# Optimization experiments

Hardware: AMD Instinct MI355X
Metric: run time of the kernel (lower is better)

The kernel has to match this reference:

```python
import jax, jax.numpy as jnp
import numpy as np

L, D, H, DR, KF = 2, 256, 8, 64, 4   # n_layer, d_model, n_head, d_rpe, k_feedforward
B, S, T = 2, 256, 256
LN_EPS = 1e-5


def _ln(x, g, b):
    m = jnp.mean(x, -1, keepdims=True)
    v = jnp.mean((x - m) ** 2, -1, keepdims=True)
    return (x - m) * jax.lax.rsqrt(v + LN_EPS) * g + b


def _attn_rpe(q_in, kv_in, rpe, tgt_mask, wq, bq, wk, bk, wv, bv, wo, bo, wr, br):
    # RPE-biased multi-head cross attention: rpe -> (rpe_k, rpe_v) added per (src,tgt) pair.
    Bq, Sq, _ = q_in.shape
    Tk = kv_in.shape[1]
    Dh = D // H
    q = (q_in @ wq + bq).reshape(Bq, Sq, H, Dh)
    k = (kv_in @ wk + bk).reshape(Bq, Tk, H, Dh)
    v = (kv_in @ wv + bv).reshape(Bq, Tk, H, Dh)
    r = rpe @ wr + br                                   # [B,S,T,2D]
    rk, rv = jnp.split(r, 2, axis=-1)
    rk = rk.reshape(Bq, Sq, Tk, H, Dh)
    rv = rv.reshape(Bq, Sq, Tk, H, Dh)
    scale = 1.0 / np.sqrt(Dh).astype(np.float32)
    scores = (jnp.einsum('bshd,bthd->bhst', q, k)
              + jnp.einsum('bshd,bsthd->bhst', q, rk)) * scale
    scores = jnp.where(tgt_mask[:, None, None, :], -jnp.inf, scores)
    w = jax.nn.softmax(scores, axis=-1)                 # [B,H,S,T]
    out = (jnp.einsum('bhst,bthd->bshd', w, v)
           + jnp.einsum('bhst,bsthd->bshd', w, rv))
    return out.reshape(Bq, Sq, D) @ wo + bo


def _forward(src, tgt, rpe, src_padding_mask, tgt_padding_mask, p):
    for i in range(L):  # loop over n_layer (structurally distinct params)
        s2 = _ln(src, p['ln1_g'][i], p['ln1_b'][i])
        tn = _ln(tgt, p['lnt_g'][i], p['lnt_b'][i])
        a = _attn_rpe(s2, tn, rpe, tgt_padding_mask,
                      p['wq'][i], p['bq'][i], p['wk'][i], p['bk'][i],
                      p['wv'][i], p['bv'][i], p['wo'][i], p['bo'][i],
                      p['wr'][i], p['br'][i])
        src = src + a
        s2 = _ln(src, p['ln2_g'][i], p['ln2_b'][i])
        s2 = jax.nn.relu(s2 @ p['w1'][i] + p['b1'][i]) @ p['w2'][i] + p['b2'][i]
        src = src + s2
        src = jnp.where(src_padding_mask[:, :, None], 0.0, src)
    return src


def setup_inputs() -> dict:
    key = jax.random.key(0)
    ks = jax.random.split(key, 16)
    f = lambda k, shp: (0.02 * jax.random.normal(k, shp)).astype(jnp.float32)
    return {
        'src': jax.random.normal(ks[0], (B, S, D), jnp.float32),
        'tgt': jax.random.normal(ks[1], (B, T, D), jnp.float32),
        'rpe': jax.random.normal(ks[2], (B, S, T, DR), jnp.float32),
        'src_padding_mask': jax.random.bernoulli(ks[3], 0.05, (B, S)),
        'tgt_padding_mask': jax.random.bernoulli(ks[4], 0.1, (B, T)),
        'ln1_g': jnp.ones((L, D), jnp.float32), 'ln1_b': jnp.zeros((L, D), jnp.float32),
        'lnt_g': jnp.ones((L, D), jnp.float32), 'lnt_b': jnp.zeros((L, D), jnp.float32),
        'ln2_g': jnp.ones((L, D), jnp.float32), 'ln2_b': jnp.zeros((L, D), jnp.float32),
        'wq': f(ks[5], (L, D, D)), 'bq': jnp.zeros((L, D), jnp.float32),
        'wk': f(ks[6], (L, D, D)), 'bk': jnp.zeros((L, D), jnp.float32),
        'wv': f(ks[7], (L, D, D)), 'bv': jnp.zeros((L, D), jnp.float32),
        'wo': f(ks[8], (L, D, D)), 'bo': jnp.zeros((L, D), jnp.float32),
        'wr': f(ks[9], (L, DR, 2 * D)), 'br': jnp.zeros((L, 2 * D), jnp.float32),
        'w1': f(ks[10], (L, D, KF * D)), 'b1': jnp.zeros((L, KF * D), jnp.float32),
        'w2': f(ks[11], (L, KF * D, D)), 'b2': jnp.zeros((L, D), jnp.float32),
    }


def reference(src, tgt, rpe, src_padding_mask, tgt_padding_mask,
              ln1_g, ln1_b, lnt_g, lnt_b, ln2_g, ln2_b,
              wq, bq, wk, bk, wv, bv, wo, bo, wr, br, w1, b1, w2, b2):
    p = dict(ln1_g=ln1_g, ln1_b=ln1_b, lnt_g=lnt_g, lnt_b=lnt_b,
             ln2_g=ln2_g, ln2_b=ln2_b, wq=wq, bq=bq, wk=wk, bk=bk,
             wv=wv, bv=bv, wo=wo, bo=bo, wr=wr, br=br,
             w1=w1, b1=b1, w2=w2, b2=b2)
    return _forward(src, tgt, rpe, src_padding_mask, tgt_padding_mask, p)
```

## Files before the change

kernel.cpp:

```cpp
#include <hip/hip_runtime.h>
#include <math.h>

#define DMODEL 256
#define NH 8
#define DH 32
#define NEG_INF -1e30f

__device__ __forceinline__ void gemm_chunk(const float (*__restrict__ As)[36],
                                           const float (*__restrict__ Bs)[64],
                                           float acc[4][4])
{
  int tid = threadIdx.x;
  int tx = tid & 15, ty = tid >> 4;
#pragma unroll 8
  for (int k = 0; k < 64; ++k) {
    float4 a  = *(const float4*)&As[k][ty * 4];
    float4 bv = *(const float4*)&Bs[k][tx * 4];
    acc[0][0] = fmaf(a.x, bv.x, acc[0][0]); acc[0][1] = fmaf(a.x, bv.y, acc[0][1]);
    acc[0][2] = fmaf(a.x, bv.z, acc[0][2]); acc[0][3] = fmaf(a.x, bv.w, acc[0][3]);
    acc[1][0] = fmaf(a.y, bv.x, acc[1][0]); acc[1][1] = fmaf(a.y, bv.y, acc[1][1]);
    acc[1][2] = fmaf(a.y, bv.z, acc[1][2]); acc[1][3] = fmaf(a.y, bv.w, acc[1][3]);
    acc[2][0] = fmaf(a.z, bv.x, acc[2][0]); acc[2][1] = fmaf(a.z, bv.y, acc[2][1]);
    acc[2][2] = fmaf(a.z, bv.z, acc[2][2]); acc[2][3] = fmaf(a.z, bv.w, acc[2][3]);
    acc[3][0] = fmaf(a.w, bv.x, acc[3][0]); acc[3][1] = fmaf(a.w, bv.y, acc[3][1]);
    acc[3][2] = fmaf(a.w, bv.z, acc[3][2]); acc[3][3] = fmaf(a.w, bv.w, acc[3][3]);
  }
}

__device__ __forceinline__ void gemm_ln(
    const float* __restrict__ Xsrc,
    const float* __restrict__ g, const float* __restrict__ b,
    const float* __restrict__ Bw, int ldb, int m0, int n0,
    float (*__restrict__ As)[64][36], float (*__restrict__ Bs)[64][64],
    float acc[4][4])
{
  int tid = threadIdx.x;
  int r = tid >> 2, p = tid & 3;
  const float* row = Xsrc + (size_t)(m0 + r) * DMODEL;
  float4 v[16];
  float s = 0.f, ss = 0.f;
#pragma unroll
  for (int j = 0; j < 16; ++j) {
    int kg = (j >> 2) * 64 + p * 16 + (j & 3) * 4;
    v[j] = *(const float4*)(row + kg);
    s  += v[j].x + v[j].y + v[j].z + v[j].w;
    ss += v[j].x * v[j].x + v[j].y * v[j].y + v[j].z * v[j].z + v[j].w * v[j].w;
  }
  s  += __shfl_xor(s, 1);  s  += __shfl_xor(s, 2);
  ss += __shfl_xor(ss, 1); ss += __shfl_xor(ss, 2);
  float mean = s * (1.0f / 256.0f);
  float var  = ss * (1.0f / 256.0f) - mean * mean;
  float rstd = rsqrtf(var + 1e-5f);
#pragma unroll
  for (int j = 0; j < 16; ++j) {
    v[j].x = (v[j].x - mean) * rstd;
    v[j].y = (v[j].y - mean) * rstd;
    v[j].z = (v[j].z - mean) * rstd;
    v[j].w = (v[j].w - mean) * rstd;
  }
#pragma unroll
  for (int i = 0; i < 8; ++i) {
    int idx = tid + 128 * i;
    int k = idx >> 4, c = (idx & 15) << 2;
    *(float4*)&Bs[0][k][c] = *(const float4*)(Bw + (size_t)k * ldb + n0 + c);
  }
#pragma unroll
  for (int j = 0; j < 4; ++j) {
    int kl = p * 16 + j * 4;
    float4 gg = *(const float4*)(g + kl);
    float4 bb = *(const float4*)(b + kl);
    As[0][kl + 0][r] = v[j].x * gg.x + bb.x;
    As[0][kl + 1][r] = v[j].y * gg.y + bb.y;
    As[0][kl + 2][r] = v[j].z * gg.z + bb.z;
    As[0][kl + 3][r] = v[j].w * gg.w + bb.w;
  }
  __syncthreads();
  for (int c = 0; c < 4; ++c) {
    int cur = c & 1;
    float4 breg[8];
    if (c < 3) {
      int kb = (c + 1) * 64;
#pragma unroll
      for (int i = 0; i < 8; ++i) {
        int idx = tid + 128 * i;
        int k = idx >> 4, cc = (idx & 15) << 2;
        breg[i] = *(const float4*)(Bw + (size_t)(kb + k) * ldb + n0 + cc);
      }
    }
    gemm_chunk(As[cur], Bs[cur], acc);
    if (c < 3) {
      int nxt = cur ^ 1;
      int kb = (c + 1) * 64;
#pragma unroll
      for (int i = 0; i < 8; ++i) {
        int idx = tid + 128 * i;
        int k = idx >> 4, cc = (idx & 15) << 2;
        *(float4*)&Bs[nxt][k][cc] = breg[i];
      }
#pragma unroll
      for (int j = 0; j < 4; ++j) {
        int kl = p * 16 + j * 4;
        float4 gg = *(const float4*)(g + kb + kl);
        float4 bb = *(const float4*)(b + kb + kl);
        float4 vv = v[(c + 1) * 4 + j];
        As[nxt][kl + 0][r] = vv.x * gg.x + bb.x;
        As[nxt][kl + 1][r] = vv.y * gg.y + bb.y;
        As[nxt][kl + 2][r] = vv.z * gg.z + bb.z;
        As[nxt][kl + 3][r] = vv.w * gg.w + bb.w;
      }
      __syncthreads();
    }
  }
}

__device__ __forceinline__ void gemm_copy(
    const float* __restrict__ A, int lda, int kbeg,
    const float* __restrict__ Bw, int ldb, int m0, int n0,
    float (*__restrict__ As)[64][36], float (*__restrict__ Bs)[64][64],
    float acc[4][4])
{
  int tid = threadIdx.x;
  int r = tid >> 2, p = tid & 3;
  const float* arow = A + (size_t)(m0 + r) * lda + kbeg;
#pragma unroll
  for (int i = 0; i < 8; ++i) {
    int idx = tid + 128 * i;
    int k = idx >> 4, c = (idx & 15) << 2;
    *(float4*)&Bs[0][k][c] = *(const float4*)(Bw + (size_t)k * ldb + n0 + c);
  }
#pragma unroll
  for (int j = 0; j < 4; ++j) {
    int kl = p * 16 + j * 4;
    float4 vv = *(const float4*)(arow + kl);
    As[0][kl + 0][r] = vv.x; As[0][kl + 1][r] = vv.y;
    As[0][kl + 2][r] = vv.z; As[0][kl + 3][r] = vv.w;
  }
  __syncthreads();
  for (int c = 0; c < 4; ++c) {
    int cur = c & 1;
    float4 breg[8]; float4 areg[4];
    if (c < 3) {
      int kb = (c + 1) * 64;
#pragma unroll
      for (int i = 0; i < 8; ++i) {
        int idx = tid + 128 * i;
        int k = idx >> 4, cc = (idx & 15) << 2;
        breg[i] = *(const float4*)(Bw + (size_t)(kb + k) * ldb + n0 + cc);
      }
#pragma unroll
      for (int j = 0; j < 4; ++j) areg[j] = *(const float4*)(arow + kb + p * 16 + j * 4);
    }
    gemm_chunk(As[cur], Bs[cur], acc);
    if (c < 3) {
      int nxt = cur ^ 1;
#pragma unroll
      for (int i = 0; i < 8; ++i) {
        int idx = tid + 128 * i;
        int k = idx >> 4, cc = (idx & 15) << 2;
        *(float4*)&Bs[nxt][k][cc] = breg[i];
      }
#pragma unroll
      for (int j = 0; j < 4; ++j) {
        int kl = p * 16 + j * 4;
        As[nxt][kl + 0][r] = areg[j].x; As[nxt][kl + 1][r] = areg[j].y;
        As[nxt][kl + 2][r] = areg[j].z; As[nxt][kl + 3][r] = areg[j].w;
      }
      __syncthreads();
    }
  }
}

__global__ __launch_bounds__(128) void qkv_kernel(
    const float* __restrict__ srcin, const float* __restrict__ tgt,
    const float* __restrict__ ln1g, const float* __restrict__ ln1b,
    const float* __restrict__ lntg, const float* __restrict__ lntb,
    const float* __restrict__ wq, const float* __restrict__ wk, const float* __restrict__ wv,
    const float* __restrict__ bq, const float* __restrict__ bk, const float* __restrict__ bv,
    float* __restrict__ Qb, float* __restrict__ Kb, float* __restrict__ Vb)
{
  __shared__ __align__(16) float As[2][64][36];
  __shared__ __align__(16) float Bs[2][64][64];
  int z = blockIdx.z;
  int m0 = blockIdx.y * 32, n0 = blockIdx.x * 64;
  const float* Bw = (z == 0) ? wq : (z == 1) ? wk : wv;
  float acc[4][4] = {};
  if (z == 0) gemm_ln(srcin, ln1g, ln1b, Bw, DMODEL, m0, n0, As, Bs, acc);
  else        gemm_ln(tgt, lntg, lntb, Bw, DMODEL, m0, n0, As, Bs, acc);
  const float* bias = (z == 0) ? bq : (z == 1) ? bk : bv;
  int tid = threadIdx.x, tx = tid & 15, ty = tid >> 4;
  int c0 = n0 + tx * 4;
  float4 bias4 = *(const float4*)(bias + c0);
  const float scale = 0.1767766952966369f;
#pragma unroll
  for (int i = 0; i < 4; ++i) {
    int m = m0 + ty * 4 + i;
    float4 r;
    r.x = acc[i][0] + bias4.x;
    r.y = acc[i][1] + bias4.y;
    r.z = acc[i][2] + bias4.z;
    r.w = acc[i][3] + bias4.w;
    if (z == 0) {
      r.x *= scale; r.y *= scale; r.z *= scale; r.w *= scale;
      *(float4*)&Qb[m * DMODEL + c0] = r;
    } else {
      int b = m >> 8, t = m & 255, h = c0 >> 5, d0 = c0 & 31;
      float* dst = ((z == 1) ? Kb : Vb) + (size_t)(b * NH + h) * 8192 + t * DH + d0;
      *(float4*)dst = r;
    }
  }
}

__global__ __launch_bounds__(128) void wo_kernel(
    const float* __restrict__ AO, const float* __restrict__ wo,
    const float* __restrict__ srcin, const float* __restrict__ bo,
    float* __restrict__ X)
{
  __shared__ __align__(16) float As[2][64][36];
  __shared__ __align__(16) float Bs[2][64][64];
  int m0 = blockIdx.y * 32, n0 = blockIdx.x * 64;
  float acc[4][4] = {};
  gemm_copy(AO, DMODEL, 0, wo, DMODEL, m0, n0, As, Bs, acc);
  int tid = threadIdx.x, tx = tid & 15, ty = tid >> 4;
  int c0 = n0 + tx * 4;
  float4 bov = *(const float4*)(bo + c0);
#pragma unroll
  for (int i = 0; i < 4; ++i) {
    int m = m0 + ty * 4 + i;
    float4 sv = *(const float4*)(srcin + (size_t)m * DMODEL + c0);
    float4 r;
    r.x = sv.x + bov.x + acc[i][0];
    r.y = sv.y + bov.y + acc[i][1];
    r.z = sv.z + bov.z + acc[i][2];
    r.w = sv.w + bov.w + acc[i][3];
    *(float4*)&X[(size_t)m * DMODEL + c0] = r;
  }
}

__global__ __launch_bounds__(128) void ff1_kernel(
    const float* __restrict__ X, const float* __restrict__ ln2g, const float* __restrict__ ln2b,
    const float* __restrict__ w1, const float* __restrict__ b1,
    const float* __restrict__ b2, const int* __restrict__ smask,
    float* __restrict__ H1, float* __restrict__ outb)
{
  __shared__ __align__(16) float As[2][64][36];
  __shared__ __align__(16) float Bs[2][64][64];
  int m0 = blockIdx.y * 32, n0 = blockIdx.x * 64;
  if (blockIdx.x == 0) {
    int tid = threadIdx.x;
    int r = tid >> 2, pq = tid & 3;
    int m = m0 + r;
    float mm = (smask[m] != 0) ? 0.0f : 1.0f;
#pragma unroll
    for (int j = 0; j < 4; ++j) {
      float4 xv  = *(const float4*)(X  + (size_t)m * DMODEL + pq * 64 + j * 16);
      float4 b2v = *(const float4*)(b2 + pq * 64 + j * 16);
      float4 o;
      o.x = mm * (xv.x + b2v.x); o.y = mm * (xv.y + b2v.y);
      o.z = mm * (xv.z + b2v.z); o.w = mm * (xv.w + b2v.w);
      *(float4*)(outb + (size_t)m * DMODEL + pq * 64 + j * 16) = o;
      float4 xv2  = *(const float4*)(X  + (size_t)m * DMODEL + pq * 64 + j * 16 + 4);
      float4 b2v2 = *(const float4*)(b2 + pq * 64 + j * 16 + 4);
      float4 o2;
      o2.x = mm * (xv2.x + b2v2.x); o2.y = mm * (xv2.y + b2v2.y);
      o2.z = mm * (xv2.z + b2v2.z); o2.w = mm * (xv2.w + b2v2.w);
      *(float4*)(outb + (size_t)m * DMODEL + pq * 64 + j * 16 + 4) = o2;
      float4 xv3  = *(const float4*)(X  + (size_t)m * DMODEL + pq * 64 + j * 16 + 8);
      float4 b2v3 = *(const float4*)(b2 + pq * 64 + j * 16 + 8);
      float4 o3;
      o3.x = mm * (xv3.x + b2v3.x); o3.y = mm * (xv3.y + b2v3.y);
      o3.z = mm * (xv3.z + b2v3.z); o3.w = mm * (xv3.w + b2v3.w);
      *(float4*)(outb + (size_t)m * DMODEL + pq * 64 + j * 16 + 8) = o3;
      float4 xv4  = *(const float4*)(X  + (size_t)m * DMODEL + pq * 64 + j * 16 + 12);
      float4 b2v4 = *(const float4*)(b2 + pq * 64 + j * 16 + 12);
      float4 o4;
      o4.x = mm * (xv4.x + b2v4.x); o4.y = mm * (xv4.y + b2v4.y);
      o4.z = mm * (xv4.z + b2v4.z); o4.w = mm * (xv4.w + b2v4.w);
      *(float4*)(outb + (size_t)m * DMODEL + pq * 64 + j * 16 + 12) = o4;
    }
  }
  float acc[4][4] = {};
  gemm_ln(X, ln2g, ln2b, w1, 1024, m0, n0, As, Bs, acc);
  int tid = threadIdx.x, tx = tid & 15, ty = tid >> 4;
  int c0 = n0 + tx * 4;
  float4 b1v = *(const float4*)(b1 + c0);
#pragma unroll
  for (int i = 0; i < 4; ++i) {
    int m = m0 + ty * 4 + i;
    float4 r;
    r.x = fmaxf(acc[i][0] + b1v.x, 0.0f);
    r.y = fmaxf(acc[i][1] + b1v.y, 0.0f);
    r.z = fmaxf(acc[i][2] + b1v.z, 0.0f);
    r.w = fmaxf(acc[i][3] + b1v.w, 0.0f);
    *(float4*)&H1[(size_t)m * 1024 + c0] = r;
  }
}

__global__ __launch_bounds__(128) void ff2_kernel(
    const float* __restrict__ H1, const float* __restrict__ w2,
    const int* __restrict__ smask, float* __restrict__ outb)
{
  __shared__ __align__(16) float As[2][64][36];
  __shared__ __align__(16) float Bs[2][64][64];
  int m0 = blockIdx.y * 32, n0 = blockIdx.x * 64;
  int kbeg = blockIdx.z * 256;
  float acc[4][4] = {};
  gemm_copy(H1, 1024, kbeg, w2 + (size_t)kbeg * DMODEL, DMODEL, m0, n0, As, Bs, acc);
  int tid = threadIdx.x, tx = tid & 15, ty = tid >> 4;
  int c0 = n0 + tx * 4;
#pragma unroll
  for (int i = 0; i < 4; ++i) {
    int m = m0 + ty * 4 + i;
    if (smask[m] == 0) {
      atomicAdd(&outb[(size_t)m * DMODEL + c0 + 0], acc[i][0]);
      atomicAdd(&outb[(size_t)m * DMODEL + c0 + 1], acc[i][1]);
      atomicAdd(&outb[(size_t)m * DMODEL + c0 + 2], acc[i][2]);
      atomicAdd(&outb[(size_t)m * DMODEL + c0 + 3], acc[i][3]);
    }
  }
}

__global__ __launch_bounds__(256) void attn_kernel(
    const float* __restrict__ Qb, const float* __restrict__ Kb, const float* __restrict__ Vb,
    const float* __restrict__ rpe, const int* __restrict__ tmask,
    const float* __restrict__ wrl, const float* __restrict__ brl,
    float* __restrict__ AO)
{
  __shared__ float Ks[256][32];
  __shared__ float Vt[32][260];
  __shared__ float ps[4][256];
  __shared__ float qs[16][32];
  __shared__ float wks[5][32];
  __shared__ float wvs[5][32];
  int bid = blockIdx.x;
  int b = bid >> 7, h = (bid >> 4) & 7, s0 = (bid & 15) << 4;
  int tid = threadIdx.x;
  const float* Kp = Kb + (size_t)(b * NH + h) * 8192;
  const float* Vp = Vb + (size_t)(b * NH + h) * 8192;
  {
    int t = tid;
    const float4* kr = (const float4*)(Kp + t * DH);
    const float4* vr = (const float4*)(Vp + t * DH);
    int sw = t & 7;
#pragma unroll
    for (int c = 0; c < 8; ++c) {
      float4 k4 = kr[c];
      *(float4*)&Ks[t][(c ^ sw) * 4] = k4;
    }
#pragma unroll
    for (int c = 0; c < 8; ++c) {
      float4 v4 = vr[c];
      Vt[c*4+0][t] = v4.x; Vt[c*4+1][t] = v4.y; Vt[c*4+2][t] = v4.z; Vt[c*4+3][t] = v4.w;
    }
  }
  if (tid < 160) {
    int j = tid >> 5, d = tid & 31;
    wks[j][d] = (j < 4) ? wrl[j * 512 + h * DH + d]       : brl[h * DH + d];
    wvs[j][d] = (j < 4) ? wrl[j * 512 + 256 + h * DH + d] : brl[256 + h * DH + d];
  }
  if (tid >= 128) {
    int u = tid - 128;
    int rr = u >> 3, cc = u & 7;
    *(float4*)&qs[rr][cc*4] =
        *(const float4*)&Qb[(b * 256 + s0 + rr) * DMODEL + h * DH + cc * 4];
  }
  __syncthreads();

  int w = tid >> 6, lane = tid & 63;
  int msk[4];
#pragma unroll
  for (int it = 0; it < 4; ++it) msk[it] = tmask[b * 256 + it * 64 + lane];

  for (int i = 0; i < 4; ++i) {
    int sl = w * 4 + i;
    int s = s0 + sl;
    float4 q4[8];
#pragma unroll
    for (int c = 0; c < 8; ++c) q4[c] = *(const float4*)&qs[sl][c * 4];
    float qw[4]; float qbr = 0.0f;
#pragma unroll
    for (int j = 0; j < 4; ++j) {
      float t0 = 0;
#pragma unroll
      for (int c = 0; c < 8; ++c) {
        float4 wv4 = *(const float4*)&wks[j][c * 4];
        t0 += q4[c].x*wv4.x + q4[c].y*wv4.y + q4[c].z*wv4.z + q4[c].w*wv4.w;
      }
      qw[j] = t0;
    }
#pragma unroll
    for (int c = 0; c < 8; ++c) {
      float4 wv4 = *(const float4*)&wks[4][c * 4];
      qbr += q4[c].x*wv4.x + q4[c].y*wv4.y + q4[c].z*wv4.z + q4[c].w*wv4.w;
    }
    const float4* rp4 = (const float4*)(rpe + (size_t)(b * 256 + s) * 1024);
    float sc[4]; float4 rr[4];
#pragma unroll
    for (int it = 0; it < 4; ++it) {
      int t = it * 64 + lane;
      int sw = t & 7;
      float sv = 0;
#pragma unroll
      for (int c = 0; c < 8; ++c) {
        float4 k4 = *(const float4*)&Ks[t][(c ^ sw) * 4];
        sv = fmaf(q4[c].x, k4.x, sv); sv = fmaf(q4[c].y, k4.y, sv);
        sv = fmaf(q4[c].z, k4.z, sv); sv = fmaf(q4[c].w, k4.w, sv);
      }
      float4 rv = rp4[t];
      rr[it] = rv;
      sv += rv.x*qw[0] + rv.y*qw[1] + rv.z*qw[2] + rv.w*qw[3] + qbr;
      if (msk[it] != 0) sv = NEG_INF;
      sc[it] = sv;
    }
    float mval = fmaxf(fmaxf(sc[0], sc[1]), fmaxf(sc[2], sc[3]));
#pragma unroll
    for (int off = 32; off >= 1; off >>= 1) mval = fmaxf(mval, __shfl_xor(mval, off));
    float p[4], lsum = 0;
#pragma unroll
    for (int it = 0; it < 4; ++it) { p[it] = __expf(sc[it] - mval); lsum += p[it]; }
    float wj0 = 0, wj1 = 0, wj2 = 0, wj3 = 0;
#pragma unroll
    for (int it = 0; it < 4; ++it) {
      wj0 = fmaf(p[it], rr[it].x, wj0);
      wj1 = fmaf(p[it], rr[it].y, wj1);
      wj2 = fmaf(p[it], rr[it].z, wj2);
      wj3 = fmaf(p[it], rr[it].w, wj3);
    }
#pragma unroll
    for (int off = 32; off >= 1; off >>= 1) {
      lsum += __shfl_xor(lsum, off);
      wj0 += __shfl_xor(wj0, off);
      wj1 += __shfl_xor(wj1, off);
      wj2 += __shfl_xor(wj2, off);
      wj3 += __shfl_xor(wj3, off);
    }
#pragma unroll
    for (int it = 0; it < 4; ++it) ps[w][it * 64 + lane] = p[it];
    int g = lane >> 5, d = lane & 31;
    float o = 0;
#pragma unroll
    for (int n = 0; n < 32; ++n) {
      int t = g * 128 + n * 4;
      float4 p4 = *(const float4*)&ps[w][t];
      float4 v4 = *(const float4*)&Vt[d][t];
      o += p4.x*v4.x + p4.y*v4.y + p4.z*v4.z + p4.w*v4.w;
    }
    o += __shfl_xor(o, 32);
    float corr = wj0 * wvs[0][d] + wj1 * wvs[1][d] + wj2 * wvs[2][d] + wj3 * wvs[3][d];
    float oval = (o + corr) / lsum + wvs[4][d];
    if (lane < 32) AO[(b * 256 + s) * DMODEL + h * DH + d] = oval;
  }
}

extern "C" void kernel_launch(void* const* d_in, const int* in_sizes, int n_in,
                              void* d_out, int out_size, void* d_ws, size_t ws_size,
                              hipStream_t stream)
{
  const float* src  = (const float*)d_in[0];
  const float* tgt  = (const float*)d_in[1];
  const float* rpe  = (const float*)d_in[2];
  const int*   smask = (const int*)d_in[3];
  const int*   tmask = (const int*)d_in[4];
  const float* ln1g = (const float*)d_in[5];
  const float* ln1b = (const float*)d_in[6];
  const float* lntg = (const float*)d_in[7];
  const float* lntb = (const float*)d_in[8];
  const float* ln2g = (const float*)d_in[9];
  const float* ln2b = (const float*)d_in[10];
  const float* wq = (const float*)d_in[11];
  const float* bq = (const float*)d_in[12];
  const float* wk = (const float*)d_in[13];
  const float* bk = (const float*)d_in[14];
  const float* wv = (const float*)d_in[15];
  const float* bv = (const float*)d_in[16];
  const float* wo = (const float*)d_in[17];
  const float* bo = (const float*)d_in[18];
  const float* wr = (const float*)d_in[19];
  const float* br = (const float*)d_in[20];
  const float* w1 = (const float*)d_in[21];
  const float* b1 = (const float*)d_in[22];
  const float* w2 = (const float*)d_in[23];
  const float* b2 = (const float*)d_in[24];

  float* w    = (float*)d_ws;
  float* Qb   = w;
  float* Kb   = w + 131072;
  float* Vb   = w + 262144;
  float* AO   = w + 393216;
  float* X    = w + 524288;
  float* SRC1 = w + 655360;
  float* H1   = w + 786432;

  for (int l = 0; l < 2; ++l) {
    const float* srcin = l ? SRC1 : src;
    float* outb = l ? (float*)d_out : SRC1;
    qkv_kernel<<<dim3(4, 16, 3), 128, 0, stream>>>(
        srcin, tgt, ln1g + l*256, ln1b + l*256, lntg + l*256, lntb + l*256,
        wq + l*65536, wk + l*65536, wv + l*65536,
        bq + l*256, bk + l*256, bv + l*256, Qb, Kb, Vb);
    attn_kernel<<<256, 256, 0, stream>>>(Qb, Kb, Vb, rpe, tmask,
                                         wr + l*2048, br + l*512, AO);
    wo_kernel<<<dim3(4, 16), 128, 0, stream>>>(AO, wo + l*65536, srcin, bo + l*256, X);
    ff1_kernel<<<dim3(16, 16), 128, 0, stream>>>(X, ln2g + l*256, ln2b + l*256,
                                                 w1 + l*262144, b1 + l*1024,
                                                 b2 + l*256, smask, H1, outb);
    ff2_kernel<<<dim3(4, 16, 4), 128, 0, stream>>>(H1, w2 + l*262144, smask, outb);
  }
}
```

Before: 271.9 us.

## Hoist layer-1 K/V projections, fuse FF1+FF2, fold residual init into Wo

K/V projections for both layers depend only on tgt, so they are now computed in one up-front launch alongside the layer-0 Q projection, and layer 1 only runs a Q-only projection. The two feed-forward GEMMs are fused: each block keeps its 64-column ReLU(H1) slice in shared memory and multiplies it by the matching W2 rows, atomically accumulating into the output. The residual plus b2 plus mask initialisation moves into the Wo epilogue. This drops the H1 global round trip and several launches (10 down to 8). The cost is more atomics per output element (16 K-splits instead of 4) and extra workspace for the second K/V set.

```diff
diff --git a/kernel.cpp b/kernel.cpp
--- a/kernel.cpp
+++ b/kernel.cpp
@@ -170,23 +170,31 @@
   }
 }
 
-__global__ __launch_bounds__(128) void qkv_kernel(
-    const float* __restrict__ srcin, const float* __restrict__ tgt,
+__global__ __launch_bounds__(128) void qkv5_kernel(
+    const float* __restrict__ src, const float* __restrict__ tgt,
     const float* __restrict__ ln1g, const float* __restrict__ ln1b,
-    const float* __restrict__ lntg, const float* __restrict__ lntb,
-    const float* __restrict__ wq, const float* __restrict__ wk, const float* __restrict__ wv,
-    const float* __restrict__ bq, const float* __restrict__ bk, const float* __restrict__ bv,
-    float* __restrict__ Qb, float* __restrict__ Kb, float* __restrict__ Vb)
+    const float* __restrict__ lntg0, const float* __restrict__ lntb0,
+    const float* __restrict__ lntg1, const float* __restrict__ lntb1,
+    const float* __restrict__ wq,  const float* __restrict__ bq,
+    const float* __restrict__ wk0, const float* __restrict__ bk0,
+    const float* __restrict__ wv0, const float* __restrict__ bv0,
+    const float* __restrict__ wk1, const float* __restrict__ bk1,
+    const float* __restrict__ wv1, const float* __restrict__ bv1,
+    float* __restrict__ Qb, float* __restrict__ Kb0, float* __restrict__ Vb0,
+    float* __restrict__ Kb1, float* __restrict__ Vb1)
 {
   __shared__ __align__(16) float As[2][64][36];
   __shared__ __align__(16) float Bs[2][64][64];
   int z = blockIdx.z;
   int m0 = blockIdx.y * 32, n0 = blockIdx.x * 64;
-  const float* Bw = (z == 0) ? wq : (z == 1) ? wk : wv;
+  const float* A  = (z == 0) ? src : tgt;
+  const float* g  = (z == 0) ? ln1g : (z <= 2) ? lntg0 : lntg1;
+  const float* bb = (z == 0) ? ln1b : (z <= 2) ? lntb0 : lntb1;
+  const float* Bw = (z == 0) ? wq : (z == 1) ? wk0 : (z == 2) ? wv0 : (z == 3) ? wk1 : wv1;
+  const float* bias = (z == 0) ? bq : (z == 1) ? bk0 : (z == 2) ? bv0 : (z == 3) ? bk1 : bv1;
+  float* dst = (z == 0) ? Qb : (z == 1) ? Kb0 : (z == 2) ? Vb0 : (z == 3) ? Kb1 : Vb1;
   float acc[4][4] = {};
-  if (z == 0) gemm_ln(srcin, ln1g, ln1b, Bw, DMODEL, m0, n0, As, Bs, acc);
-  else        gemm_ln(tgt, lntg, lntb, Bw, DMODEL, m0, n0, As, Bs, acc);
-  const float* bias = (z == 0) ? bq : (z == 1) ? bk : bv;
+  gemm_ln(A, g, bb, Bw, DMODEL, m0, n0, As, Bs, acc);
   int tid = threadIdx.x, tx = tid & 15, ty = tid >> 4;
   int c0 = n0 + tx * 4;
   float4 bias4 = *(const float4*)(bias + c0);
@@ -201,19 +209,46 @@
     r.w = acc[i][3] + bias4.w;
     if (z == 0) {
       r.x *= scale; r.y *= scale; r.z *= scale; r.w *= scale;
-      *(float4*)&Qb[m * DMODEL + c0] = r;
+      *(float4*)&dst[m * DMODEL + c0] = r;
     } else {
       int b = m >> 8, t = m & 255, h = c0 >> 5, d0 = c0 & 31;
-      float* dst = ((z == 1) ? Kb : Vb) + (size_t)(b * NH + h) * 8192 + t * DH + d0;
-      *(float4*)dst = r;
-    }
+      *(float4*)&dst[(size_t)(b * NH + h) * 8192 + t * DH + d0] = r;
+    }
+  }
+}
+
+__global__ __launch_bounds__(128) void q_kernel(
+    const float* __restrict__ srcin,
+    const float* __restrict__ ln1g, const float* __restrict__ ln1b,
+    const float* __restrict__ wq, const float* __restrict__ bq,
+    float* __restrict__ Qb)
+{
+  __shared__ __align__(16) float As[2][64][36];
+  __shared__ __align__(16) float Bs[2][64][64];
+  int m0 = blockIdx.y * 32, n0 = blockIdx.x * 64;
+  float acc[4][4] = {};
+  gemm_ln(srcin, ln1g, ln1b, wq, DMODEL, m0, n0, As, Bs, acc);
+  int tid = threadIdx.x, tx = tid & 15, ty = tid >> 4;
+  int c0 = n0 + tx * 4;
+  float4 bias4 = *(const float4*)(bq + c0);
+  const float scale = 0.1767766952966369f;
+#pragma unroll
+  for (int i = 0; i < 4; ++i) {
+    int m = m0 + ty * 4 + i;
+    float4 r;
+    r.x = (acc[i][0] + bias4.x) * scale;
+    r.y = (acc[i][1] + bias4.y) * scale;
+    r.z = (acc[i][2] + bias4.z) * scale;
+    r.w = (acc[i][3] + bias4.w) * scale;
+    *(float4*)&Qb[m * DMODEL + c0] = r;
   }
 }
 
 __global__ __launch_bounds__(128) void wo_kernel(
     const float* __restrict__ AO, const float* __restrict__ wo,
     const float* __restrict__ srcin, const float* __restrict__ bo,
-    float* __restrict__ X)
+    const float* __restrict__ b2, const int* __restrict__ smask,
+    float* __restrict__ X, float* __restrict__ outb)
 {
   __shared__ __align__(16) float As[2][64][36];
   __shared__ __align__(16) float Bs[2][64][64];
@@ -223,6 +258,7 @@
   int tid = threadIdx.x, tx = tid & 15, ty = tid >> 4;
   int c0 = n0 + tx * 4;
   float4 bov = *(const float4*)(bo + c0);
+  float4 b2v = *(const float4*)(b2 + c0);
 #pragma unroll
   for (int i = 0; i < 4; ++i) {
     int m = m0 + ty * 4 + i;
@@ -233,88 +269,81 @@
     r.z = sv.z + bov.z + acc[i][2];
     r.w = sv.w + bov.w + acc[i][3];
     *(float4*)&X[(size_t)m * DMODEL + c0] = r;
-  }
-}
-
-__global__ __launch_bounds__(128) void ff1_kernel(
+    float mm = (smask[m] != 0) ? 0.0f : 1.0f;
+    float4 o;
+    o.x = mm * (r.x + b2v.x); o.y = mm * (r.y + b2v.y);
+    o.z = mm * (r.z + b2v.z); o.w = mm * (r.w + b2v.w);
+    *(float4*)&outb[(size_t)m * DMODEL + c0] = o;
+  }
+}
+
+__global__ __launch_bounds__(128) void ff_fused_kernel(
     const float* __restrict__ X, const float* __restrict__ ln2g, const float* __restrict__ ln2b,
     const float* __restrict__ w1, const float* __restrict__ b1,
-    const float* __restrict__ b2, const int* __restrict__ smask,
-    float* __restrict__ H1, float* __restrict__ outb)
+    const float* __restrict__ w2, const int* __restrict__ smask,
+    float* __restrict__ outb)
 {
   __shared__ __align__(16) float As[2][64][36];
   __shared__ __align__(16) float Bs[2][64][64];
-  int m0 = blockIdx.y * 32, n0 = blockIdx.x * 64;
-  if (blockIdx.x == 0) {
-    int tid = threadIdx.x;
-    int r = tid >> 2, pq = tid & 3;
-    int m = m0 + r;
-    float mm = (smask[m] != 0) ? 0.0f : 1.0f;
-#pragma unroll
-    for (int j = 0; j < 4; ++j) {
-      float4 xv  = *(const float4*)(X  + (size_t)m * DMODEL + pq * 64 + j * 16);
-      float4 b2v = *(const float4*)(b2 + pq * 64 + j * 16);
-      float4 o;
-      o.x = mm * (xv.x + b2v.x); o.y = mm * (xv.y + b2v.y);
-      o.z = mm * (xv.z + b2v.z); o.w = mm * (xv.w + b2v.w);
-      *(float4*)(outb + (size_t)m * DMODEL + pq * 64 + j * 16) = o;
-      float4 xv2  = *(const float4*)(X  + (size_t)m * DMODEL + pq * 64 + j * 16 + 4);
-      float4 b2v2 = *(const float4*)(b2 + pq * 64 + j * 16 + 4);
-      float4 o2;
-      o2.x = mm * (xv2.x + b2v2.x); o2.y = mm * (xv2.y + b2v2.y);
-      o2.z = mm * (xv2.z + b2v2.z); o2.w = mm * (xv2.w + b2v2.w);
-      *(float4*)(outb + (size_t)m * DMODEL + pq * 64 + j * 16 + 4) = o2;
-      float4 xv3  = *(const float4*)(X  + (size_t)m * DMODEL + pq * 64 + j * 16 + 8);
-      float4 b2v3 = *(const float4*)(b2 + pq * 64 + j * 16 + 8);
-      float4 o3;
-      o3.x = mm * (xv3.x + b2v3.x); o3.y = mm * (xv3.y + b2v3.y);
-      o3.z = mm * (xv3.z + b2v3.z); o3.w = mm * (xv3.w + b2v3.w);
-      *(float4*)(outb + (size_t)m * DMODEL + pq * 64 + j * 16 + 8) = o3;
-      float4 xv4  = *(const float4*)(X  + (size_t)m * DMODEL + pq * 64 + j * 16 + 12);
-      float4 b2v4 = *(const float4*)(b2 + pq * 64 + j * 16 + 12);
-      float4 o4;
-      o4.x = mm * (xv4.x + b2v4.x); o4.y = mm * (xv4.y + b2v4.y);
-      o4.z = mm * (xv4.z + b2v4.z); o4.w = mm * (xv4.w + b2v4.w);
-      *(float4*)(outb + (size_t)m * DMODEL + pq * 64 + j * 16 + 12) = o4;
-    }
-  }
+  __shared__ __align__(16) float H1t[64][36];
+  int m0 = blockIdx.y * 32;
+  int ks = blockIdx.x * 64;
   float acc[4][4] = {};
-  gemm_ln(X, ln2g, ln2b, w1, 1024, m0, n0, As, Bs, acc);
+  gemm_ln(X, ln2g, ln2b, w1, 1024, m0, ks, As, Bs, acc);
   int tid = threadIdx.x, tx = tid & 15, ty = tid >> 4;
-  int c0 = n0 + tx * 4;
-  float4 b1v = *(const float4*)(b1 + c0);
+  float4 b1v = *(const float4*)(b1 + ks + tx * 4);
 #pragma unroll
   for (int i = 0; i < 4; ++i) {
-    int m = m0 + ty * 4 + i;
-    float4 r;
-    r.x = fmaxf(acc[i][0] + b1v.x, 0.0f);
-    r.y = fmaxf(acc[i][1] + b1v.y, 0.0f);
-    r.z = fmaxf(acc[i][2] + b1v.z, 0.0f);
-    r.w = fmaxf(acc[i][3] + b1v.w, 0.0f);
-    *(float4*)&H1[(size_t)m * 1024 + c0] = r;
-  }
-}
-
-__global__ __launch_bounds__(128) void ff2_kernel(
-    const float* __restrict__ H1, const float* __restrict__ w2,
-    const int* __restrict__ smask, float* __restrict__ outb)
-{
-  __shared__ __align__(16) float As[2][64][36];
-  __shared__ __align__(16) float Bs[2][64][64];
-  int m0 = blockIdx.y * 32, n0 = blockIdx.x * 64;
-  int kbeg = blockIdx.z * 256;
-  float acc[4][4] = {};
-  gemm_copy(H1, 1024, kbeg, w2 + (size_t)kbeg * DMODEL, DMODEL, m0, n0, As, Bs, acc);
-  int tid = threadIdx.x, tx = tid & 15, ty = tid >> 4;
-  int c0 = n0 + tx * 4;
-#pragma unroll
-  for (int i = 0; i < 4; ++i) {
-    int m = m0 + ty * 4 + i;
-    if (smask[m] == 0) {
-      atomicAdd(&outb[(size_t)m * DMODEL + c0 + 0], acc[i][0]);
-      atomicAdd(&outb[(size_t)m * DMODEL + c0 + 1], acc[i][1]);
-      atomicAdd(&outb[(size_t)m * DMODEL + c0 + 2], acc[i][2]);
-      atomicAdd(&outb[(size_t)m * DMODEL + c0 + 3], acc[i][3]);
+    H1t[tx * 4 + 0][ty * 4 + i] = fmaxf(acc[i][0] + b1v.x, 0.0f);
+    H1t[tx * 4 + 1][ty * 4 + i] = fmaxf(acc[i][1] + b1v.y, 0.0f);
+    H1t[tx * 4 + 2][ty * 4 + i] = fmaxf(acc[i][2] + b1v.z, 0.0f);
+    H1t[tx * 4 + 3][ty * 4 + i] = fmaxf(acc[i][3] + b1v.w, 0.0f);
+  }
+  const float* w2s = w2 + (size_t)ks * DMODEL;
+#pragma unroll
+  for (int i = 0; i < 8; ++i) {
+    int idx = tid + 128 * i;
+    int k = idx >> 4, c = (idx & 15) << 2;
+    *(float4*)&Bs[0][k][c] = *(const float4*)(w2s + (size_t)k * DMODEL + c);
+  }
+  __syncthreads();
+  int msk[4];
+#pragma unroll
+  for (int i = 0; i < 4; ++i) msk[i] = smask[m0 + ty * 4 + i];
+  for (int nc = 0; nc < 4; ++nc) {
+    int cur = nc & 1;
+    float4 breg[8];
+    if (nc < 3) {
+      int nb = (nc + 1) * 64;
+#pragma unroll
+      for (int i = 0; i < 8; ++i) {
+        int idx = tid + 128 * i;
+        int k = idx >> 4, c = (idx & 15) << 2;
+        breg[i] = *(const float4*)(w2s + (size_t)k * DMODEL + nb + c);
+      }
+    }
+    float a2[4][4] = {};
+    gemm_chunk(H1t, Bs[cur], a2);
+    int c0 = nc * 64 + tx * 4;
+#pragma unroll
+    for (int i = 0; i < 4; ++i) {
+      int m = m0 + ty * 4 + i;
+      if (msk[i] == 0) {
+        atomicAdd(&outb[(size_t)m * DMODEL + c0 + 0], a2[i][0]);
+        atomicAdd(&outb[(size_t)m * DMODEL + c0 + 1], a2[i][1]);
+        atomicAdd(&outb[(size_t)m * DMODEL + c0 + 2], a2[i][2]);
+        atomicAdd(&outb[(size_t)m * DMODEL + c0 + 3], a2[i][3]);
+      }
+    }
+    if (nc < 3) {
+      int nxt = cur ^ 1;
+#pragma unroll
+      for (int i = 0; i < 8; ++i) {
+        int idx = tid + 128 * i;
+        int k = idx >> 4, c = (idx & 15) << 2;
+        *(float4*)&Bs[nxt][k][c] = breg[i];
+      }
+      __syncthreads();
     }
   }
 }
@@ -483,26 +512,29 @@
 
   float* w    = (float*)d_ws;
   float* Qb   = w;
-  float* Kb   = w + 131072;
-  float* Vb   = w + 262144;
-  float* AO   = w + 393216;
-  float* X    = w + 524288;
-  float* SRC1 = w + 655360;
-  float* H1   = w + 786432;
-
-  for (int l = 0; l < 2; ++l) {
-    const float* srcin = l ? SRC1 : src;
-    float* outb = l ? (float*)d_out : SRC1;
-    qkv_kernel<<<dim3(4, 16, 3), 128, 0, stream>>>(
-        srcin, tgt, ln1g + l*256, ln1b + l*256, lntg + l*256, lntb + l*256,
-        wq + l*65536, wk + l*65536, wv + l*65536,
-        bq + l*256, bk + l*256, bv + l*256, Qb, Kb, Vb);
-    attn_kernel<<<256, 256, 0, stream>>>(Qb, Kb, Vb, rpe, tmask,
-                                         wr + l*2048, br + l*512, AO);
-    wo_kernel<<<dim3(4, 16), 128, 0, stream>>>(AO, wo + l*65536, srcin, bo + l*256, X);
-    ff1_kernel<<<dim3(16, 16), 128, 0, stream>>>(X, ln2g + l*256, ln2b + l*256,
-                                                 w1 + l*262144, b1 + l*1024,
-                                                 b2 + l*256, smask, H1, outb);
-    ff2_kernel<<<dim3(4, 16, 4), 128, 0, stream>>>(H1, w2 + l*262144, smask, outb);
-  }
-}
+  float* Kb0  = w + 131072;
+  float* Vb0  = w + 262144;
+  float* Kb1  = w + 393216;
+  float* Vb1  = w + 524288;
+  float* AO   = w + 655360;
+  float* X    = w + 786432;
+  float* SRC1 = w + 917504;
+
+  qkv5_kernel<<<dim3(4, 16, 5), 128, 0, stream>>>(
+      src, tgt, ln1g, ln1b, lntg, lntb, lntg + 256, lntb + 256,
+      wq, bq, wk, bk, wv, bv, wk + 65536, bk + 256, wv + 65536, bv + 256,
+      Qb, Kb0, Vb0, Kb1, Vb1);
+  attn_kernel<<<256, 256, 0, stream>>>(Qb, Kb0, Vb0, rpe, tmask, wr, br, AO);
+  wo_kernel<<<dim3(4, 16), 128, 0, stream>>>(AO, wo, src, bo, b2, smask, X, SRC1);
+  ff_fused_kernel<<<dim3(16, 16), 128, 0, stream>>>(X, ln2g, ln2b, w1, b1, w2,
+                                                    smask, SRC1);
+  q_kernel<<<dim3(4, 16), 128, 0, stream>>>(SRC1, ln1g + 256, ln1b + 256,
+                                            wq + 65536, bq + 256, Qb);
+  attn_kernel<<<256, 256, 0, stream>>>(Qb, Kb1, Vb1, rpe, tmask,
+                                       wr + 2048, br + 512, AO);
+  wo_kernel<<<dim3(4, 16), 128, 0, stream>>>(AO, wo + 65536, SRC1, bo + 256,
+                                             b2 + 256, smask, X, (float*)d_out);
+  ff_fused_kernel<<<dim3(16, 16), 128, 0, stream>>>(X, ln2g + 256, ln2b + 256,
+                                                    w1 + 262144, b1 + 1024,
+                                                    w2 + 262144, smask, (float*)d_out);
+}
```

After: 292.6 us. 1.08x slower.
